# Kernel optimization log

Hardware: AMD Instinct MI355X
Metric: run time of the kernel (lower is better)

Reference implementation:

```python
import math
import jax, jax.numpy as jnp
import numpy as np

D = 768
H = 12
HD = D // H  # 64


def setup_inputs() -> dict:
    key = jax.random.key(0)
    ks = jax.random.split(key, 12)
    B, S = 4, 1024
    s = 0.02
    return {
        "q": jax.random.normal(ks[0], (B, S, D), jnp.float32),
        "k": jax.random.normal(ks[1], (B, S, D), jnp.float32),
        "v": jax.random.normal(ks[2], (B, S, D), jnp.float32),
        # nn.Linear weights are [out, in]; y = x @ W.T + b
        "Wq": jax.random.normal(ks[3], (D, D), jnp.float32) * s,
        "bq": jnp.zeros((D,), jnp.float32),
        "Wl": jax.random.normal(ks[4], (H, H), jnp.float32) * 0.3,  # logits_proj
        "bl": jnp.zeros((H,), jnp.float32),
        "Wp": jax.random.normal(ks[5], (H, H), jnp.float32) * 0.3,  # weights_proj
        "bp": jnp.zeros((H,), jnp.float32),
        "Wf": jax.random.normal(ks[6], (D, D), jnp.float32) * s,    # fcc_layer
        "bf": jnp.zeros((D,), jnp.float32),
    }


def reference(q, k, v, Wq, bq, Wl, bl, Wp, bp, Wf, bf):
    B, S, _ = q.shape

    # NOTE: original code applies self.query to q, k AND v (faithful quirk).
    def proj(x):
        return (x @ Wq.T + bq).reshape(B, S, H, HD).transpose(0, 2, 1, 3)  # [B,H,S,HD]

    qh, kh, vh = proj(q), proj(k), proj(v)

    logits = jnp.einsum("bhqd,bhkd->bhqk", qh, kh) / math.sqrt(HD)  # [B,H,S,S]
    # talking-heads pre-softmax mix: Linear over head axis (transpose(1,-1) trick)
    logits = jnp.einsum("bhqk,gh->bgqk", logits, Wl) + bl[None, :, None, None]

    attn = jax.nn.softmax(logits, axis=-1)  # dropout is identity in eval
    # talking-heads post-softmax mix
    attn = jnp.einsum("bhqk,gh->bgqk", attn, Wp) + bp[None, :, None, None]

    out = jnp.einsum("bhqk,bhkd->bhqd", attn, vh)  # [B,H,S,HD]
    out = out.transpose(0, 2, 1, 3).reshape(B, S, D)
    return out @ Wf.T + bf
```

## Files before the change

### kernel.cpp

```cpp
#include <hip/hip_runtime.h>
#include <hip/hip_bf16.h>

typedef short bf16x8 __attribute__((ext_vector_type(8)));
typedef short bf16x4 __attribute__((ext_vector_type(4)));
typedef float f32x4 __attribute__((ext_vector_type(4)));

#define MFMA16(a,b,c) __builtin_amdgcn_mfma_f32_16x16x32_bf16(a,b,c,0,0,0)

__device__ __forceinline__ unsigned short f2bf(float x){
    unsigned int u = __float_as_uint(x);
    u += 0x7fffu + ((u >> 16) & 1u);
    return (unsigned short)(u >> 16);
}
__device__ __forceinline__ float bf2f(unsigned short h){
    return __uint_as_float(((unsigned int)h) << 16);
}
__device__ __forceinline__ unsigned int f2bf2(float a, float b){
    return ((unsigned int)f2bf(a)) | (((unsigned int)f2bf(b)) << 16);
}

__global__ __launch_bounds__(256) void gemm_proj(
    const float* __restrict__ Aq, const float* __restrict__ Ak, const float* __restrict__ Av,
    const float* __restrict__ W, const float* __restrict__ bias,
    unsigned short* __restrict__ qh, unsigned short* __restrict__ kh,
    unsigned short* __restrict__ vt)
{
    __shared__ __align__(16) unsigned short As[128][56];
    __shared__ __align__(16) unsigned short Bs[64][56];
    const int z = blockIdx.z;
    const float* A = (z == 0) ? Aq : ((z == 1) ? Ak : Av);
    const int m0 = blockIdx.x * 128, n0 = blockIdx.y * 64;
    const int tid = threadIdx.x;
    const int w = tid >> 6, lane = tid & 63, col15 = lane & 15, quad = lane >> 4;

    f32x4 c[2][4];
#pragma unroll
    for (int ms = 0; ms < 2; ++ms)
#pragma unroll
        for (int ns = 0; ns < 4; ++ns) c[ms][ns] = (f32x4){0.f, 0.f, 0.f, 0.f};

    const int arow = tid >> 1, acol = (tid & 1) * 16;
    const int brow = tid >> 2, bcol = (tid & 3) * 8;

    for (int k0 = 0; k0 < 768; k0 += 32) {
        __syncthreads();
        {
            const float* s = A + (size_t)(m0 + arow) * 768 + k0 + acol;
            float4 f0 = ((const float4*)s)[0], f1 = ((const float4*)s)[1];
            float4 f2 = ((const float4*)s)[2], f3 = ((const float4*)s)[3];
            uint4 w0 = make_uint4(f2bf2(f0.x, f0.y), f2bf2(f0.z, f0.w),
                                  f2bf2(f1.x, f1.y), f2bf2(f1.z, f1.w));
            uint4 w1 = make_uint4(f2bf2(f2.x, f2.y), f2bf2(f2.z, f2.w),
                                  f2bf2(f3.x, f3.y), f2bf2(f3.z, f3.w));
            *(uint4*)&As[arow][acol] = w0;
            *(uint4*)&As[arow][acol + 8] = w1;
        }
        {
            const float* s = W + (size_t)(n0 + brow) * 768 + k0 + bcol;
            float4 f0 = ((const float4*)s)[0], f1 = ((const float4*)s)[1];
            uint4 w0 = make_uint4(f2bf2(f0.x, f0.y), f2bf2(f0.z, f0.w),
                                  f2bf2(f1.x, f1.y), f2bf2(f1.z, f1.w));
            *(uint4*)&Bs[brow][bcol] = w0;
        }
        __syncthreads();
        bf16x8 af0 = *(const bf16x8*)&As[w * 32 + col15][quad * 8];
        bf16x8 af1 = *(const bf16x8*)&As[w * 32 + 16 + col15][quad * 8];
        bf16x8 b0 = *(const bf16x8*)&Bs[col15][quad * 8];
        bf16x8 b1 = *(const bf16x8*)&Bs[16 + col15][quad * 8];
        bf16x8 b2 = *(const bf16x8*)&Bs[32 + col15][quad * 8];
        bf16x8 b3 = *(const bf16x8*)&Bs[48 + col15][quad * 8];
        c[0][0] = MFMA16(af0, b0, c[0][0]);
        c[0][1] = MFMA16(af0, b1, c[0][1]);
        c[0][2] = MFMA16(af0, b2, c[0][2]);
        c[0][3] = MFMA16(af0, b3, c[0][3]);
        c[1][0] = MFMA16(af1, b0, c[1][0]);
        c[1][1] = MFMA16(af1, b1, c[1][1]);
        c[1][2] = MFMA16(af1, b2, c[1][2]);
        c[1][3] = MFMA16(af1, b3, c[1][3]);
    }

#pragma unroll
    for (int ms = 0; ms < 2; ++ms)
#pragma unroll
        for (int ns = 0; ns < 4; ++ns) {
            const int colg = n0 + ns * 16 + col15;
            const float bv = bias[colg];
            const int h = colg >> 6, d = colg & 63;
#pragma unroll
            for (int e = 0; e < 4; ++e) {
                const int m = m0 + w * 32 + ms * 16 + quad * 4 + e;
                const int b = m >> 10, sIdx = m & 1023;
                const float val = c[ms][ns][e] + bv;
                if (z == 2)
                    vt[((b * 12 + h) * 64 + d) * 1024 + sIdx] = f2bf(val);
                else {
                    unsigned short* dst = (z == 0) ? qh : kh;
                    dst[((b * 12 + h) * 1024 + sIdx) * 64 + d] = f2bf(val);
                }
            }
        }
}

__global__ __launch_bounds__(256) void gemm_out(
    const unsigned short* __restrict__ Abf, const float* __restrict__ W,
    const float* __restrict__ bias, float* __restrict__ out)
{
    __shared__ __align__(16) unsigned short As[128][56];
    __shared__ __align__(16) unsigned short Bs[64][56];
    const int m0 = blockIdx.x * 128, n0 = blockIdx.y * 64;
    const int tid = threadIdx.x;
    const int w = tid >> 6, lane = tid & 63, col15 = lane & 15, quad = lane >> 4;

    f32x4 c[2][4];
#pragma unroll
    for (int ms = 0; ms < 2; ++ms)
#pragma unroll
        for (int ns = 0; ns < 4; ++ns) c[ms][ns] = (f32x4){0.f, 0.f, 0.f, 0.f};

    const int arow = tid >> 1, acol = (tid & 1) * 16;
    const int brow = tid >> 2, bcol = (tid & 3) * 8;

    for (int k0 = 0; k0 < 768; k0 += 32) {
        __syncthreads();
        {
            const unsigned short* s = Abf + (size_t)(m0 + arow) * 768 + k0 + acol;
            *(bf16x8*)&As[arow][acol] = *(const bf16x8*)s;
            *(bf16x8*)&As[arow][acol + 8] = *(const bf16x8*)(s + 8);
        }
        {
            const float* s = W + (size_t)(n0 + brow) * 768 + k0 + bcol;
            float4 f0 = ((const float4*)s)[0], f1 = ((const float4*)s)[1];
            uint4 w0 = make_uint4(f2bf2(f0.x, f0.y), f2bf2(f0.z, f0.w),
                                  f2bf2(f1.x, f1.y), f2bf2(f1.z, f1.w));
            *(uint4*)&Bs[brow][bcol] = w0;
        }
        __syncthreads();
        bf16x8 af0 = *(const bf16x8*)&As[w * 32 + col15][quad * 8];
        bf16x8 af1 = *(const bf16x8*)&As[w * 32 + 16 + col15][quad * 8];
        bf16x8 b0 = *(const bf16x8*)&Bs[col15][quad * 8];
        bf16x8 b1 = *(const bf16x8*)&Bs[16 + col15][quad * 8];
        bf16x8 b2 = *(const bf16x8*)&Bs[32 + col15][quad * 8];
        bf16x8 b3 = *(const bf16x8*)&Bs[48 + col15][quad * 8];
        c[0][0] = MFMA16(af0, b0, c[0][0]);
        c[0][1] = MFMA16(af0, b1, c[0][1]);
        c[0][2] = MFMA16(af0, b2, c[0][2]);
        c[0][3] = MFMA16(af0, b3, c[0][3]);
        c[1][0] = MFMA16(af1, b0, c[1][0]);
        c[1][1] = MFMA16(af1, b1, c[1][1]);
        c[1][2] = MFMA16(af1, b2, c[1][2]);
        c[1][3] = MFMA16(af1, b3, c[1][3]);
    }

#pragma unroll
    for (int ms = 0; ms < 2; ++ms)
#pragma unroll
        for (int ns = 0; ns < 4; ++ns) {
            const int colg = n0 + ns * 16 + col15;
            const float bv = bias[colg];
#pragma unroll
            for (int e = 0; e < 4; ++e) {
                const int m = m0 + w * 32 + ms * 16 + quad * 4 + e;
                out[(size_t)m * 768 + colg] = c[ms][ns][e] + bv;
            }
        }
}

__global__ __launch_bounds__(256) void colsum_k(
    const unsigned short* __restrict__ vt, float* __restrict__ cs)
{
    const int row = blockIdx.x * 4 + (threadIdx.x >> 6);
    const int lane = threadIdx.x & 63;
    const unsigned short* p = vt + (size_t)row * 1024;
    float s = 0.f;
    for (int i = lane; i < 1024; i += 64) s += bf2f(p[i]);
    s += __shfl_xor(s, 1, 64);  s += __shfl_xor(s, 2, 64);
    s += __shfl_xor(s, 4, 64);  s += __shfl_xor(s, 8, 64);
    s += __shfl_xor(s, 16, 64); s += __shfl_xor(s, 32, 64);
    if (lane == 0) cs[row] = s;
}

__device__ __forceinline__ bf16x8 make_mix_frag(const float* __restrict__ Wm,
                                                int col15, int quad, float scale)
{
    bf16x8 f;
#pragma unroll
    for (int j = 0; j < 8; ++j) {
        const int kk = quad * 8 + j;
        float v = (col15 < 12 && kk < 12) ? Wm[col15 * 12 + kk] * scale : 0.f;
        f[j] = (short)f2bf(v);
    }
    return f;
}

__device__ __forceinline__ bf16x8 lds_afrag(const unsigned short* rp)
{
    bf16x4 lo = *(const bf16x4*)rp;
    bf16x4 hi = *(const bf16x4*)(rp + 4);
    return (bf16x8){lo[0], lo[1], lo[2], lo[3], hi[0], hi[1], hi[2], hi[3]};
}

__global__ __launch_bounds__(256) void attn_pass1(
    const unsigned short* __restrict__ qh, const unsigned short* __restrict__ kh,
    const float* __restrict__ Wl, const float* __restrict__ bl,
    float* __restrict__ l_part)
{
    const int ks = blockIdx.x, qt = blockIdx.y, b = blockIdx.z;
    const int tid = threadIdx.x, w = tid >> 6, lane = tid & 63;
    const int col15 = lane & 15, quad = lane >> 4;
    const int q0 = qt * 16;

    __shared__ __align__(16) unsigned short Sm1[4 * 5128];
    __shared__ float lred[4][16][16];

    unsigned short* sm = Sm1 + w * 5128;
#pragma unroll
    for (int r = 0; r < 4; ++r)
        *(uint2*)&sm[(r * 64 + lane) * 20 + 12] = make_uint2(0u, 0u);

    const bf16x8 wlf = make_mix_frag(Wl, col15, quad, 0.125f);
    const float blv = (col15 < 12) ? bl[col15] : 0.f;
    const f32x4 cinit = (f32x4){blv, blv, blv, blv};

    const unsigned short* qbase = qh + (size_t)(b * 12) * 65536 + (size_t)(q0 + col15) * 64 + quad * 8;
    const unsigned short* kbase0 = kh + (size_t)(b * 12) * 65536 + (size_t)(ks * 512 + w * 16 + col15) * 64 + quad * 8;

    float lsum[16];
#pragma unroll
    for (int t = 0; t < 16; ++t) lsum[t] = 0.f;

    for (int it = 0; it < 8; ++it) {
        const unsigned short* kbase = kbase0 + it * 64 * 64;
#pragma unroll
        for (int hp = 0; hp < 6; ++hp) {
            const int h0 = hp * 2;
            const unsigned short* qp0 = qbase + (size_t)h0 * 65536;
            const unsigned short* kp0 = kbase + (size_t)h0 * 65536;
            f32x4 s0 = (f32x4){0.f, 0.f, 0.f, 0.f};
            f32x4 s1 = (f32x4){0.f, 0.f, 0.f, 0.f};
            s0 = MFMA16(*(const bf16x8*)qp0, *(const bf16x8*)kp0, s0);
            s0 = MFMA16(*(const bf16x8*)(qp0 + 32), *(const bf16x8*)(kp0 + 32), s0);
            s1 = MFMA16(*(const bf16x8*)(qp0 + 65536), *(const bf16x8*)(kp0 + 65536), s1);
            s1 = MFMA16(*(const bf16x8*)(qp0 + 65568), *(const bf16x8*)(kp0 + 65568), s1);
#pragma unroll
            for (int e = 0; e < 4; ++e) {
                const int elem = (quad * 4 + e) * 16 + col15;
                *(unsigned int*)&sm[elem * 20 + h0] = f2bf2(s0[e], s1[e]);
            }
        }
#pragma unroll
        for (int half = 0; half < 2; ++half) {
            f32x4 m[8];
#pragma unroll
            for (int t8 = 0; t8 < 8; ++t8) {
                const int t = half * 8 + t8;
                m[t8] = MFMA16(lds_afrag(sm + (t * 16 + col15) * 20 + (quad & 1) * 8),
                               wlf, cinit);
            }
#pragma unroll
            for (int t8 = 0; t8 < 8; ++t8)
                lsum[half * 8 + t8] += __expf(m[t8][0]) + __expf(m[t8][1])
                                     + __expf(m[t8][2]) + __expf(m[t8][3]);
        }
    }

    if (true) {
#pragma unroll
        for (int t = 0; t < 16; ++t) {
            float s = lsum[t];
            s += __shfl_xor(s, 16, 64);
            s += __shfl_xor(s, 32, 64);
            lsum[t] = s;
        }
    }
    if (quad == 0) {
#pragma unroll
        for (int t = 0; t < 16; ++t) lred[w][col15][t] = lsum[t];
    }
    __syncthreads();
    if (tid < 192) {
        const int g = tid >> 4, r = tid & 15;
        const float tot = lred[0][g][r] + lred[1][g][r] + lred[2][g][r] + lred[3][g][r];
        l_part[((size_t)(ks * 4 + b) * 12 + g) * 1024 + q0 + r] = tot;
    }
}

__global__ __launch_bounds__(256) void attn_pass2(
    const unsigned short* __restrict__ qh, const unsigned short* __restrict__ kh,
    const unsigned short* __restrict__ vt,
    const float* __restrict__ Wl, const float* __restrict__ bl,
    const float* __restrict__ Wp,
    const float* __restrict__ l_part, float* __restrict__ attn_part)
{
    const int ks = blockIdx.x, qt = blockIdx.y, b = blockIdx.z;
    const int tid = threadIdx.x, w = tid >> 6, lane = tid & 63;
    const int col15 = lane & 15, quad = lane >> 4;
    const int q0 = qt * 16;

    __shared__ __align__(16) unsigned short Sm1[4 * 5128];
    __shared__ __align__(16) unsigned short Pt[12][16][72];
    __shared__ float linvs[16][16];

    unsigned short* sm = Sm1 + w * 5128;
#pragma unroll
    for (int r = 0; r < 4; ++r)
        *(uint2*)&sm[(r * 64 + lane) * 20 + 12] = make_uint2(0u, 0u);

    {
        const int g = tid >> 4, r = tid & 15;
        float vv = 1.f;
        if (g < 12) {
            const float s = l_part[((size_t)(0 + b) * 12 + g) * 1024 + q0 + r]
                          + l_part[((size_t)(4 + b) * 12 + g) * 1024 + q0 + r];
            vv = 1.f / s;
        }
        linvs[g][r] = vv;
    }

    const bf16x8 wlf = make_mix_frag(Wl, col15, quad, 0.125f);
    const bf16x8 wpf = make_mix_frag(Wp, col15, quad, 1.0f);
    const float blv = (col15 < 12) ? bl[col15] : 0.f;
    const f32x4 cinit = (f32x4){blv, blv, blv, blv};
    const f32x4 zf = (f32x4){0.f, 0.f, 0.f, 0.f};

    __syncthreads();
    float linvv[16];
#pragma unroll
    for (int t = 0; t < 16; ++t) linvv[t] = linvs[col15][t];

    const unsigned short* qbase = qh + (size_t)(b * 12) * 65536 + (size_t)(q0 + col15) * 64 + quad * 8;
    const unsigned short* kbase0 = kh + (size_t)(b * 12) * 65536 + (size_t)(ks * 512 + w * 16 + col15) * 64 + quad * 8;
    const unsigned short* vbase0 = vt + (size_t)(b * 12) * 65536 + (size_t)col15 * 1024 + ks * 512 + quad * 8;

    f32x4 of[3][4];
#pragma unroll
    for (int i = 0; i < 3; ++i)
#pragma unroll
        for (int ds = 0; ds < 4; ++ds) of[i][ds] = zf;

    for (int pt = 0; pt < 8; ++pt) {
        const unsigned short* kbase = kbase0 + pt * 64 * 64;

#pragma unroll
        for (int hp = 0; hp < 6; ++hp) {
            const int h0 = hp * 2;
            const unsigned short* qp0 = qbase + (size_t)h0 * 65536;
            const unsigned short* kp0 = kbase + (size_t)h0 * 65536;
            f32x4 s0 = zf, s1 = zf;
            s0 = MFMA16(*(const bf16x8*)qp0, *(const bf16x8*)kp0, s0);
            s0 = MFMA16(*(const bf16x8*)(qp0 + 32), *(const bf16x8*)(kp0 + 32), s0);
            s1 = MFMA16(*(const bf16x8*)(qp0 + 65536), *(const bf16x8*)(kp0 + 65536), s1);
            s1 = MFMA16(*(const bf16x8*)(qp0 + 65568), *(const bf16x8*)(kp0 + 65568), s1);
#pragma unroll
            for (int e = 0; e < 4; ++e) {
                const int elem = (quad * 4 + e) * 16 + col15;
                *(unsigned int*)&sm[elem * 20 + h0] = f2bf2(s0[e], s1[e]);
            }
        }

#pragma unroll
        for (int half = 0; half < 2; ++half) {
            f32x4 m[8];
#pragma unroll
            for (int t8 = 0; t8 < 8; ++t8) {
                const int t = half * 8 + t8;
                m[t8] = MFMA16(lds_afrag(sm + (t * 16 + col15) * 20 + (quad & 1) * 8),
                               wlf, cinit);
            }
#pragma unroll
            for (int t8 = 0; t8 < 8; ++t8) {
                const int t = half * 8 + t8;
                const float li = linvv[t];
#pragma unroll
                for (int e = 0; e < 4; ++e)
                    sm[(t * 16 + quad * 4 + e) * 20 + col15] = f2bf(__expf(m[t8][e]) * li);
            }
#pragma unroll
            for (int t8 = 0; t8 < 8; ++t8) {
                const int t = half * 8 + t8;
                f32x4 o = MFMA16(lds_afrag(sm + (t * 16 + col15) * 20 + (quad & 1) * 8),
                                 wpf, zf);
                if (col15 < 12) {
                    uint2 pk = make_uint2(f2bf2(o[0], o[1]), f2bf2(o[2], o[3]));
                    *(uint2*)&Pt[col15][t][w * 16 + quad * 4] = pk;
                }
            }
        }
        __syncthreads();

#pragma unroll
        for (int i = 0; i < 3; ++i) {
            const int g2 = w * 3 + i;
            const unsigned short* vb = vbase0 + (size_t)g2 * 65536 + pt * 64;
#pragma unroll
            for (int ksub = 0; ksub < 2; ++ksub) {
                bf16x8 afp = *(const bf16x8*)&Pt[g2][col15][ksub * 32 + quad * 8];
#pragma unroll
                for (int ds = 0; ds < 4; ++ds) {
                    bf16x8 bv = *(const bf16x8*)(vb + (size_t)ds * 16384 + ksub * 32);
                    of[i][ds] = MFMA16(afp, bv, of[i][ds]);
                }
            }
        }
        __syncthreads();
    }

#pragma unroll
    for (int i = 0; i < 3; ++i) {
        const int g2 = w * 3 + i;
#pragma unroll
        for (int ds = 0; ds < 4; ++ds) {
            const int colg = g2 * 64 + ds * 16 + col15;
#pragma unroll
            for (int e = 0; e < 4; ++e) {
                const int m = b * 1024 + q0 + quad * 4 + e;
                attn_part[(size_t)ks * 3145728 + (size_t)m * 768 + colg] = of[i][ds][e];
            }
        }
    }
}

__global__ __launch_bounds__(256) void cvt2_k(
    const float* __restrict__ ap, const float* __restrict__ cs,
    const float* __restrict__ bp, unsigned short* __restrict__ abf)
{
    const int idx = blockIdx.x * 256 + threadIdx.x;
    float v = ap[idx] + ap[idx + 3145728];
    const int col = idx % 768;
    const int b = idx / 786432;
    const int g = col >> 6, d = col & 63;
    v += bp[g] * cs[(b * 12 + g) * 64 + d];
    abf[idx] = f2bf(v);
}

extern "C" void kernel_launch(void* const* d_in, const int* in_sizes, int n_in,
                              void* d_out, int out_size, void* d_ws, size_t ws_size,
                              hipStream_t stream)
{
    const float* q  = (const float*)d_in[0];
    const float* k  = (const float*)d_in[1];
    const float* v  = (const float*)d_in[2];
    const float* Wq = (const float*)d_in[3];
    const float* bq = (const float*)d_in[4];
    const float* Wl = (const float*)d_in[5];
    const float* bl = (const float*)d_in[6];
    const float* Wp = (const float*)d_in[7];
    const float* bp = (const float*)d_in[8];
    const float* Wf = (const float*)d_in[9];
    const float* bfv = (const float*)d_in[10];

    char* ws = (char*)d_ws;
    unsigned short* qh   = (unsigned short*)(ws);
    unsigned short* kh   = (unsigned short*)(ws + 6291456);
    unsigned short* vt   = (unsigned short*)(ws + 12582912);
    float*          lpart= (float*)(ws + 18874368);
    float*          csum = (float*)(ws + 19267584);
    unsigned short* abf  = (unsigned short*)(ws + 19279872);
    float*          apart= (float*)(ws + 25571328);
    float* outp = (float*)d_out;

    hipLaunchKernelGGL(gemm_proj, dim3(32, 12, 3), dim3(256), 0, stream,
                       q, k, v, Wq, bq, qh, kh, vt);
    hipLaunchKernelGGL(colsum_k, dim3(768), dim3(256), 0, stream, vt, csum);
    hipLaunchKernelGGL(attn_pass1, dim3(2, 64, 4), dim3(256), 0, stream,
                       qh, kh, Wl, bl, lpart);
    hipLaunchKernelGGL(attn_pass2, dim3(2, 64, 4), dim3(256), 0, stream,
                       qh, kh, vt, Wl, bl, Wp, lpart, apart);
    hipLaunchKernelGGL(cvt2_k, dim3(12288), dim3(256), 0, stream,
                       apart, csum, bp, abf);
    hipLaunchKernelGGL(gemm_out, dim3(32, 12), dim3(256), 0, stream,
                       abf, Wf, bfv, outp);
}
```

Measured before the change: 445.2 us.

## Template attention passes on key-split count and split keys four ways

Attention pass1/pass2 and the partial-sum reduction are templated on the number of key splits, and split count 4 is used when the workspace is large enough, doubling grid size so more blocks fill the GPU. Launch bounds now request 3 blocks per CU. Pass2's softmax/mix loop is restructured to process one 16-key tile at a time through a small per-wave LDS buffer instead of batching 8 tiles, which is meant to reduce register pressure. The cost is more partial outputs to write and reduce in cvt2_k, plus extra reads of qh for each split.

```diff
diff --git a/kernel.cpp b/kernel.cpp
--- a/kernel.cpp
+++ b/kernel.cpp
@@ -199,7 +199,8 @@
     return (bf16x8){lo[0], lo[1], lo[2], lo[3], hi[0], hi[1], hi[2], hi[3]};
 }
 
-__global__ __launch_bounds__(256) void attn_pass1(
+template<int KS>
+__global__ __launch_bounds__(256, 3) void attn_pass1(
     const unsigned short* __restrict__ qh, const unsigned short* __restrict__ kh,
     const float* __restrict__ Wl, const float* __restrict__ bl,
     float* __restrict__ l_part)
@@ -208,6 +209,7 @@
     const int tid = threadIdx.x, w = tid >> 6, lane = tid & 63;
     const int col15 = lane & 15, quad = lane >> 4;
     const int q0 = qt * 16;
+    const int keys0 = ks * (1024 / KS);
 
     __shared__ __align__(16) unsigned short Sm1[4 * 5128];
     __shared__ float lred[4][16][16];
@@ -222,13 +224,13 @@
     const f32x4 cinit = (f32x4){blv, blv, blv, blv};
 
     const unsigned short* qbase = qh + (size_t)(b * 12) * 65536 + (size_t)(q0 + col15) * 64 + quad * 8;
-    const unsigned short* kbase0 = kh + (size_t)(b * 12) * 65536 + (size_t)(ks * 512 + w * 16 + col15) * 64 + quad * 8;
+    const unsigned short* kbase0 = kh + (size_t)(b * 12) * 65536 + (size_t)(keys0 + w * 16 + col15) * 64 + quad * 8;
 
     float lsum[16];
 #pragma unroll
     for (int t = 0; t < 16; ++t) lsum[t] = 0.f;
 
-    for (int it = 0; it < 8; ++it) {
+    for (int it = 0; it < 16 / KS; ++it) {
         const unsigned short* kbase = kbase0 + it * 64 * 64;
 #pragma unroll
         for (int hp = 0; hp < 6; ++hp) {
@@ -263,14 +265,12 @@
         }
     }
 
-    if (true) {
-#pragma unroll
-        for (int t = 0; t < 16; ++t) {
-            float s = lsum[t];
-            s += __shfl_xor(s, 16, 64);
-            s += __shfl_xor(s, 32, 64);
-            lsum[t] = s;
-        }
+#pragma unroll
+    for (int t = 0; t < 16; ++t) {
+        float s = lsum[t];
+        s += __shfl_xor(s, 16, 64);
+        s += __shfl_xor(s, 32, 64);
+        lsum[t] = s;
     }
     if (quad == 0) {
 #pragma unroll
@@ -284,7 +284,8 @@
     }
 }
 
-__global__ __launch_bounds__(256) void attn_pass2(
+template<int KS>
+__global__ __launch_bounds__(256, 3) void attn_pass2(
     const unsigned short* __restrict__ qh, const unsigned short* __restrict__ kh,
     const unsigned short* __restrict__ vt,
     const float* __restrict__ Wl, const float* __restrict__ bl,
@@ -295,12 +296,16 @@
     const int tid = threadIdx.x, w = tid >> 6, lane = tid & 63;
     const int col15 = lane & 15, quad = lane >> 4;
     const int q0 = qt * 16;
+    const int keys0 = ks * (1024 / KS);
 
     __shared__ __align__(16) unsigned short Sm1[4 * 5128];
+    __shared__ __align__(16) unsigned short Sm2[4 * 328];
     __shared__ __align__(16) unsigned short Pt[12][16][72];
     __shared__ float linvs[16][16];
 
     unsigned short* sm = Sm1 + w * 5128;
+    unsigned short* sm2 = Sm2 + w * 328;
+
 #pragma unroll
     for (int r = 0; r < 4; ++r)
         *(uint2*)&sm[(r * 64 + lane) * 20 + 12] = make_uint2(0u, 0u);
@@ -309,8 +314,10 @@
         const int g = tid >> 4, r = tid & 15;
         float vv = 1.f;
         if (g < 12) {
-            const float s = l_part[((size_t)(0 + b) * 12 + g) * 1024 + q0 + r]
-                          + l_part[((size_t)(4 + b) * 12 + g) * 1024 + q0 + r];
+            float s = 0.f;
+#pragma unroll
+            for (int sp = 0; sp < KS; ++sp)
+                s += l_part[((size_t)(sp * 4 + b) * 12 + g) * 1024 + q0 + r];
             vv = 1.f / s;
         }
         linvs[g][r] = vv;
@@ -328,8 +335,8 @@
     for (int t = 0; t < 16; ++t) linvv[t] = linvs[col15][t];
 
     const unsigned short* qbase = qh + (size_t)(b * 12) * 65536 + (size_t)(q0 + col15) * 64 + quad * 8;
-    const unsigned short* kbase0 = kh + (size_t)(b * 12) * 65536 + (size_t)(ks * 512 + w * 16 + col15) * 64 + quad * 8;
-    const unsigned short* vbase0 = vt + (size_t)(b * 12) * 65536 + (size_t)col15 * 1024 + ks * 512 + quad * 8;
+    const unsigned short* kbase0 = kh + (size_t)(b * 12) * 65536 + (size_t)(keys0 + w * 16 + col15) * 64 + quad * 8;
+    const unsigned short* vbase0 = vt + (size_t)(b * 12) * 65536 + (size_t)col15 * 1024 + keys0 + quad * 8;
 
     f32x4 of[3][4];
 #pragma unroll
@@ -337,7 +344,7 @@
 #pragma unroll
         for (int ds = 0; ds < 4; ++ds) of[i][ds] = zf;
 
-    for (int pt = 0; pt < 8; ++pt) {
+    for (int pt = 0; pt < 16 / KS; ++pt) {
         const unsigned short* kbase = kbase0 + pt * 64 * 64;
 
 #pragma unroll
@@ -358,31 +365,20 @@
         }
 
 #pragma unroll
-        for (int half = 0; half < 2; ++half) {
-            f32x4 m[8];
-#pragma unroll
-            for (int t8 = 0; t8 < 8; ++t8) {
-                const int t = half * 8 + t8;
-                m[t8] = MFMA16(lds_afrag(sm + (t * 16 + col15) * 20 + (quad & 1) * 8),
-                               wlf, cinit);
-            }
-#pragma unroll
-            for (int t8 = 0; t8 < 8; ++t8) {
-                const int t = half * 8 + t8;
-                const float li = linvv[t];
-#pragma unroll
-                for (int e = 0; e < 4; ++e)
-                    sm[(t * 16 + quad * 4 + e) * 20 + col15] = f2bf(__expf(m[t8][e]) * li);
-            }
-#pragma unroll
-            for (int t8 = 0; t8 < 8; ++t8) {
-                const int t = half * 8 + t8;
-                f32x4 o = MFMA16(lds_afrag(sm + (t * 16 + col15) * 20 + (quad & 1) * 8),
-                                 wpf, zf);
-                if (col15 < 12) {
-                    uint2 pk = make_uint2(f2bf2(o[0], o[1]), f2bf2(o[2], o[3]));
-                    *(uint2*)&Pt[col15][t][w * 16 + quad * 4] = pk;
-                }
+        for (int t = 0; t < 16; ++t) {
+            f32x4 m = MFMA16(lds_afrag(sm + (t * 16 + col15) * 20 + (quad & 1) * 8),
+                             wlf, cinit);
+            const float li = linvv[t];
+#pragma unroll
+            for (int e = 0; e < 4; ++e) {
+                const float p = __expf(m[e]) * li;
+                sm2[(quad * 4 + e) * 20 + col15] = f2bf(p);
+            }
+            f32x4 o = MFMA16(lds_afrag(sm2 + col15 * 20 + (quad & 1) * 8),
+                             wpf, zf);
+            if (col15 < 12) {
+                uint2 pk = make_uint2(f2bf2(o[0], o[1]), f2bf2(o[2], o[3]));
+                *(uint2*)&Pt[col15][t][w * 16 + quad * 4] = pk;
             }
         }
         __syncthreads();
@@ -419,12 +415,15 @@
     }
 }
 
+template<int KS>
 __global__ __launch_bounds__(256) void cvt2_k(
     const float* __restrict__ ap, const float* __restrict__ cs,
     const float* __restrict__ bp, unsigned short* __restrict__ abf)
 {
     const int idx = blockIdx.x * 256 + threadIdx.x;
-    float v = ap[idx] + ap[idx + 3145728];
+    float v = 0.f;
+#pragma unroll
+    for (int sp = 0; sp < KS; ++sp) v += ap[idx + (size_t)sp * 3145728];
     const int col = idx % 768;
     const int b = idx / 786432;
     const int g = col >> 6, d = col & 63;
@@ -453,20 +452,32 @@
     unsigned short* kh   = (unsigned short*)(ws + 6291456);
     unsigned short* vt   = (unsigned short*)(ws + 12582912);
     float*          lpart= (float*)(ws + 18874368);
-    float*          csum = (float*)(ws + 19267584);
-    unsigned short* abf  = (unsigned short*)(ws + 19279872);
-    float*          apart= (float*)(ws + 25571328);
+    float*          csum = (float*)(ws + 19660800);
+    unsigned short* abf  = (unsigned short*)(ws + 19673088);
+    float*          apart= (float*)(ws + 25964544);
     float* outp = (float*)d_out;
 
     hipLaunchKernelGGL(gemm_proj, dim3(32, 12, 3), dim3(256), 0, stream,
                        q, k, v, Wq, bq, qh, kh, vt);
     hipLaunchKernelGGL(colsum_k, dim3(768), dim3(256), 0, stream, vt, csum);
-    hipLaunchKernelGGL(attn_pass1, dim3(2, 64, 4), dim3(256), 0, stream,
-                       qh, kh, Wl, bl, lpart);
-    hipLaunchKernelGGL(attn_pass2, dim3(2, 64, 4), dim3(256), 0, stream,
-                       qh, kh, vt, Wl, bl, Wp, lpart, apart);
-    hipLaunchKernelGGL(cvt2_k, dim3(12288), dim3(256), 0, stream,
-                       apart, csum, bp, abf);
+
+    const bool big = ws_size >= (size_t)25964544 + 4ull * 12582912ull;
+    if (big) {
+        hipLaunchKernelGGL((attn_pass1<4>), dim3(4, 64, 4), dim3(256), 0, stream,
+                           qh, kh, Wl, bl, lpart);
+        hipLaunchKernelGGL((attn_pass2<4>), dim3(4, 64, 4), dim3(256), 0, stream,
+                           qh, kh, vt, Wl, bl, Wp, lpart, apart);
+        hipLaunchKernelGGL((cvt2_k<4>), dim3(12288), dim3(256), 0, stream,
+                           apart, csum, bp, abf);
+    } else {
+        hipLaunchKernelGGL((attn_pass1<2>), dim3(2, 64, 4), dim3(256), 0, stream,
+                           qh, kh, Wl, bl, lpart);
+        hipLaunchKernelGGL((attn_pass2<2>), dim3(2, 64, 4), dim3(256), 0, stream,
+                           qh, kh, vt, Wl, bl, Wp, lpart, apart);
+        hipLaunchKernelGGL((cvt2_k<2>), dim3(12288), dim3(256), 0, stream,
+                           apart, csum, bp, abf);
+    }
+
     hipLaunchKernelGGL(gemm_out, dim3(32, 12), dim3(256), 0, stream,
                        abf, Wf, bfv, outp);
 }
```

Measured after the change: 452.3 us. About the same (+1.6%).
